# Kernel tuning notes

Measured on AMD Instinct MI355X. Metric: run time of the kernel, lower is better.

## Reference

```python
import jax, jax.numpy as jnp
import numpy as np

N_EMBD = 1024
N_HEAD = 16
HEAD_DIM = N_EMBD // N_HEAD
BLOCK_SIZE = 2048
ROPE_BASE = 10000.0


def _rope_tables(dim, max_len, base=ROPE_BASE):
    half = dim // 2
    freqs = 1.0 / base ** (jnp.arange(half, dtype=jnp.float32) / half)
    angles = jnp.arange(max_len, dtype=jnp.float32)[:, None] * freqs[None, :]  # (T, half)
    return jnp.cos(angles), jnp.sin(angles)


def _apply_rope(x, cos, sin):
    # x: (B, H, T, D); cos/sin: (T, D//2)
    T = x.shape[2]
    c = cos[:T][None, None]
    s = sin[:T][None, None]
    x1 = x[..., ::2]
    x2 = x[..., 1::2]
    out = jnp.stack([x1 * c - x2 * s, x1 * s + x2 * c], axis=-1)  # (B,H,T,D//2,2)
    return out.reshape(x.shape)


def setup_inputs() -> dict:
    key = jax.random.key(0)
    k1, k2, k3, k4, k5 = jax.random.split(key, 5)
    B, T, C = 2, 2048, N_EMBD
    x = jax.random.normal(k1, (B, T, C), dtype=jnp.float32)
    scale = 1.0 / np.sqrt(C)
    Wqkv = jax.random.normal(k2, (C, 3 * C), dtype=jnp.float32) * scale
    bqkv = jax.random.normal(k3, (3 * C,), dtype=jnp.float32) * 0.01
    Wproj = jax.random.normal(k4, (C, C), dtype=jnp.float32) * scale
    bproj = jax.random.normal(k5, (C,), dtype=jnp.float32) * 0.01
    cos, sin = _rope_tables(HEAD_DIM, BLOCK_SIZE)
    return {"x": x, "Wqkv": Wqkv, "bqkv": bqkv, "Wproj": Wproj, "bproj": bproj,
            "cos": cos, "sin": sin}


def reference(x, Wqkv, bqkv, Wproj, bproj, cos, sin):
    B, T, C = x.shape
    H, D = N_HEAD, HEAD_DIM
    qkv = x @ Wqkv + bqkv  # (B,T,3C)
    q, k, v = jnp.split(qkv, 3, axis=-1)
    # (B,T,C) -> (B,H,T,D)
    q = q.reshape(B, T, H, D).transpose(0, 2, 1, 3)
    k = k.reshape(B, T, H, D).transpose(0, 2, 1, 3)
    v = v.reshape(B, T, H, D).transpose(0, 2, 1, 3)
    q = _apply_rope(q, cos, sin)
    k = _apply_rope(k, cos, sin)
    att = jnp.einsum('bhtd,bhsd->bhts', q, k) * (D ** -0.5)
    causal = jnp.tril(jnp.ones((T, T), dtype=bool))
    att = jnp.where(causal[None, None], att, -jnp.inf)
    att = jax.nn.softmax(att, axis=-1)
    y = jnp.einsum('bhts,bhsd->bhtd', att, v)  # (B,H,T,D)
    y = y.transpose(0, 2, 1, 3).reshape(B, T, C)
    return y @ Wproj + bproj
```

## Files before the change

kernel.cpp:

```cpp
#include <hip/hip_runtime.h>
#include <stdint.h>

typedef short s16x8 __attribute__((ext_vector_type(8)));
typedef float f32x4 __attribute__((ext_vector_type(4)));
typedef unsigned short u16;
typedef unsigned int u32;

__device__ __forceinline__ float bf2f(u16 u) {
  union { u32 i; float f; } v; v.i = ((u32)u) << 16; return v.f;
}
__device__ __forceinline__ u16 f2bf(float f) {
  union { float f; u32 i; } v; v.f = f;
  u32 i = v.i;
  return (u16)((i + 0x7fffu + ((i >> 16) & 1u)) >> 16);
}
__device__ __forceinline__ u16 f2bf_fast(float f) {
  union { float f; u32 i; } v; v.f = f;
  return (u16)((v.i + 0x8000u) >> 16);
}

__device__ __forceinline__ s16x8 load8(const void* p, size_t idx, int isf32) {
  s16x8 r;
  if (isf32) {
    const float* f = (const float*)p + idx;
    f32x4 a = *(const f32x4*)f;
    f32x4 b = *(const f32x4*)(f + 4);
#pragma unroll
    for (int j = 0; j < 4; j++) {
      r[j] = (short)f2bf(a[j]);
      r[4 + j] = (short)f2bf(b[j]);
    }
  } else {
    r = *(const s16x8*)((const u16*)p + idx);
  }
  return r;
}
__device__ __forceinline__ float loadf(const void* p, size_t idx, int isf32) {
  return isf32 ? ((const float*)p)[idx] : bf2f(((const u16*)p)[idx]);
}

__device__ __forceinline__ void cp16(const u16* g, u16* l) {
  __builtin_amdgcn_global_load_lds(
      (const __attribute__((address_space(1))) u32*)g,
      (__attribute__((address_space(3))) u32*)l, 16, 0, 0);
}

__global__ void detect_dtype(const u16* __restrict__ x, int* __restrict__ flags) {
  int cnt = 0;
  for (int i = threadIdx.x; i < 4096; i += 64) {
    int e = (x[i] >> 7) & 0xFF;
    if (e >= 0xF0) cnt++;
  }
  unsigned long long any = __ballot(cnt > 0);
  if (threadIdx.x == 0) {
    flags[0] = (any != 0ull) ? 1 : 0;
    flags[1] = 0;
  }
}

__global__ __launch_bounds__(256) void convert_x(const void* __restrict__ x,
                                                 const int* __restrict__ fp,
                                                 u16* __restrict__ xb) {
  int tid = blockIdx.x * 256 + threadIdx.x;
  int r = tid & 127, kq = (tid >> 7) & 3, kB = (tid >> 9) & 31, mB = tid >> 14;
  size_t src = (size_t)(mB * 128 + r) * 1024 + kB * 32 + kq * 8;
  *(s16x8*)(xb + (size_t)tid * 8) = load8(x, src, *fp);
}

__global__ __launch_bounds__(256) void transposeW2(
    const void* __restrict__ Wqkv, const void* __restrict__ Wproj,
    const int* __restrict__ fp, u16* __restrict__ WqkvT,
    u16* __restrict__ WprojT) {
  __shared__ u32 tile32[32 * 66];
  const int f = *fp;
  const int tid = threadIdx.x;
  const int bx = blockIdx.x;
  const void* W;
  u16* WT;
  int N, nb, qkvSide;
  if (bx < 48) { W = Wqkv; WT = WqkvT; N = 3072; nb = bx * 64; qkvSide = 1; }
  else         { W = Wproj; WT = WprojT; N = 1024; nb = (bx - 48) * 64; qkvSide = 0; }
  const int kb = blockIdx.y * 64;
  {
    int a = tid >> 3, c8 = tid & 7;
    s16x8 r0 = load8(W, (size_t)(kb + 2 * a) * N + nb + c8 * 8, f);
    s16x8 r1 = load8(W, (size_t)(kb + 2 * a + 1) * N + nb + c8 * 8, f);
#pragma unroll
    for (int j = 0; j < 8; j++)
      tile32[a * 66 + c8 * 8 + j] = (u32)(u16)r0[j] | ((u32)(u16)r1[j] << 16);
  }
  __syncthreads();
#pragma unroll
  for (int i = 0; i < 2; i++) {
    int idx = tid + i * 256;
    int n = idx & 63, c8 = idx >> 6;
    s16x8 v;
#pragma unroll
    for (int w = 0; w < 4; w++) {
      u32 pk = tile32[(c8 * 4 + w) * 66 + n];
      v[2 * w] = (short)(u16)(pk & 0xFFFF);
      v[2 * w + 1] = (short)(u16)(pk >> 16);
    }
    int R = nb + n, k = kb + c8 * 8;
    int kB = k >> 5, kq = (k >> 3) & 3;
    size_t off;
    if (qkvSide) {
      int nB = R >> 7, r = R & 127;
      off = ((size_t)(nB * 32 + kB) * 4 + kq) * 1024 + r * 8;
    } else {
      int nB = R >> 6, r = R & 63;
      off = (size_t)(nB * 32 + kB) * 2048 + kq * 512 + r * 8;
    }
    *(s16x8*)(WT + off) = v;
  }
}

__global__ __launch_bounds__(256) void transposeV(const u16* __restrict__ qkv,
                                                  u16* __restrict__ vT) {
  __shared__ u32 tile32[64 * 33];
  const int tid = threadIdx.x;
  const int tb = blockIdx.x * 64, bh = blockIdx.y;
  const int b = bh >> 4, h = bh & 15;
  {
    int a = tid >> 3, c8 = tid & 7;
    const u16* base = qkv + (size_t)(b * 2048 + tb + 2 * a) * 3072 + 2048 + h * 64;
    s16x8 r0 = *(const s16x8*)(base + c8 * 8);
    s16x8 r1 = *(const s16x8*)(base + 3072 + c8 * 8);
#pragma unroll
    for (int j = 0; j < 8; j++)
      tile32[(c8 * 8 + j) * 33 + a] = (u32)(u16)r0[j] | ((u32)(u16)r1[j] << 16);
  }
  __syncthreads();
#pragma unroll
  for (int i = 0; i < 2; i++) {
    int idx = tid + i * 256;
    int d = idx >> 3, c8 = idx & 7;
    s16x8 v;
#pragma unroll
    for (int w = 0; w < 4; w++) {
      u32 pk = tile32[d * 33 + c8 * 4 + w];
      v[2 * w] = (short)(u16)(pk & 0xFFFF);
      v[2 * w + 1] = (short)(u16)(pk >> 16);
    }
    *(s16x8*)(vT + ((size_t)bh * 64 + d) * 2048 + tb + c8 * 8) = v;
  }
}

template <int MB, int NT, int KK, int ATILED>
__global__ __launch_bounds__(256, 6) void gemm_bt(
    const u16* __restrict__ A, int lda, const u16* __restrict__ Bt,
    const void* __restrict__ bias, const int* __restrict__ fI32,
    void* __restrict__ C, int ropeMode, int outF,
    const void* __restrict__ cost, const void* __restrict__ sint, int N) {
  constexpr int MT = MB / 32;
  constexpr int NTW = NT / 32;
  constexpr int KT = KK / 32;
  constexpr int APW = MB / 64;
  constexpr int BPW = NT / 64;
  __shared__ __attribute__((aligned(16))) u16 As[MB * 32];
  __shared__ __attribute__((aligned(16))) u16 Bs[NT * 32];
  const int inf32 = *fI32;
  const int tid = threadIdx.x;
  const int wave = tid >> 6, lane = tid & 63, quad = lane >> 4, l16 = lane & 15;
  const int bx = blockIdx.x, by = blockIdx.y;
  const int m0 = by * MB, n0 = bx * NT;
  const int wm = (wave & 1) * (MB / 2), wn = (wave >> 1) * (NT / 2);
  f32x4 acc[MT][NTW];
#pragma unroll
  for (int i = 0; i < MT; i++)
#pragma unroll
    for (int j = 0; j < NTW; j++) acc[i][j] = (f32x4){0.f, 0.f, 0.f, 0.f};

  const u16* aT = nullptr;
  const u16* aP = nullptr;
  int halfA = 0;
  if constexpr (ATILED) {
    const int mB = (MB == 128) ? by : (by >> 1);
    halfA = (MB == 128) ? 0 : (by & 1);
    aT = A + (size_t)mB * KK * 128 + lane * 8;
  } else {
    const int lr = lane >> 2, lk = (lane & 3) * 8;
    aP = A + (size_t)(m0 + wave * (MB / 4) + lr) * lda + lk;
  }
  const u16* bT = Bt + (size_t)bx * KK * NT + lane * 8;

  for (int s = 0; s < KT; ++s) {
    __syncthreads();
    if constexpr (ATILED) {
#pragma unroll
      for (int j = 0; j < APW; j++) {
        const int c = wave * APW + j;
        size_t off;
        if constexpr (MB == 128) off = (size_t)s * 4096 + c * 512;
        else                     off = (size_t)s * 4096 + c * 1024 + halfA * 512;
        cp16(aT + off, As + c * 512);
      }
    } else {
      const int kb = s * 32;
#pragma unroll
      for (int j = 0; j < APW; j++)
        cp16(aP + kb + (size_t)(16 * j) * lda, As + wave * (APW * 512) + j * 512);
    }
#pragma unroll
    for (int j = 0; j < BPW; j++) {
      const int c = wave * BPW + j;
      cp16(bT + (size_t)s * (NT * 32) + c * 512, Bs + c * 512);
    }
    __syncthreads();
    s16x8 af[MT], bfr[NTW];
#pragma unroll
    for (int mt = 0; mt < MT; mt++) {
      if constexpr (ATILED)
        af[mt] = *(const s16x8*)(As + quad * (MB * 8) + (wm + mt * 16 + l16) * 8);
      else
        af[mt] = *(const s16x8*)(As + (wm + mt * 16 + l16) * 32 + quad * 8);
    }
#pragma unroll
    for (int nt = 0; nt < NTW; nt++)
      bfr[nt] = *(const s16x8*)(Bs + quad * (NT * 8) + (wn + nt * 16 + l16) * 8);
#pragma unroll
    for (int mt = 0; mt < MT; mt++)
#pragma unroll
      for (int nt = 0; nt < NTW; nt++)
        acc[mt][nt] = __builtin_amdgcn_mfma_f32_16x16x32_bf16(
            af[mt], bfr[nt], acc[mt][nt], 0, 0, 0);
  }

#pragma unroll
  for (int nt = 0; nt < NTW; nt++) {
    int col = n0 + wn + nt * 16 + l16;
    float bv = loadf(bias, col, inf32);
    if (ropeMode && col < 2048) {
      int j = (col & 63) >> 1, odd = col & 1;
#pragma unroll
      for (int mt = 0; mt < MT; mt++)
#pragma unroll
        for (int r = 0; r < 4; r++) {
          int row = m0 + wm + mt * 16 + quad * 4 + r, t = row & 2047;
          float cv = loadf(cost, (size_t)t * 32 + j, inf32);
          float sv = loadf(sint, (size_t)t * 32 + j, inf32);
          float val = acc[mt][nt][r] + bv;
          float pr = __shfl_xor(val, 1);
          float res = odd ? (pr * sv + val * cv) : (val * cv - pr * sv);
          ((u16*)C)[(size_t)row * N + col] = f2bf(res);
        }
    } else if (outF && inf32) {
#pragma unroll
      for (int mt = 0; mt < MT; mt++)
#pragma unroll
        for (int r = 0; r < 4; r++) {
          int row = m0 + wm + mt * 16 + quad * 4 + r;
          ((float*)C)[(size_t)row * N + col] = acc[mt][nt][r] + bv;
        }
    } else {
#pragma unroll
      for (int mt = 0; mt < MT; mt++)
#pragma unroll
        for (int r = 0; r < 4; r++) {
          int row = m0 + wm + mt * 16 + quad * 4 + r;
          ((u16*)C)[(size_t)row * N + col] = f2bf(acc[mt][nt][r] + bv);
        }
    }
  }
}

__device__ __forceinline__ int kvIdx(int chunk, int row) {
  return chunk * 512 + (((row & 56) | ((row ^ chunk) & 7)) << 3);
}
__device__ __forceinline__ int pIdx(int chunk, int row) {
  return chunk * 128 + (((row & 8) | ((row ^ chunk) & 7)) << 3);
}

__global__ __launch_bounds__(512) void attn_kernel(u16* qkv,
                                                   const u16* __restrict__ vT) {
  __shared__ __attribute__((aligned(16))) u16 Ks[8 * 512];
  __shared__ __attribute__((aligned(16))) u16 Vt[8 * 512];
  __shared__ __attribute__((aligned(16))) u16 Pl[8][8 * 128];
  const int tid = threadIdx.x;
  const int wave = tid >> 6, lane = tid & 63, quad = lane >> 4, l16 = lane & 15;
  const int cu = blockIdx.x & 255, round = blockIdx.x >> 8;
  const int p = cu >> 5, bh = cu & 31;
  const int qt = round ? p : 15 - p;
  const int h = bh & 15;
  const size_t rb = (size_t)(bh >> 4) * 2048;
  const int qb = qt * 128;
  const float SCALE = 0.18033688011112042f;

  s16x8 qa0, qa1;
  {
    const u16* qp = qkv + (rb + qb + wave * 16 + l16) * 3072 + h * 64;
    qa0 = *(const s16x8*)(qp + quad * 8);
    qa1 = *(const s16x8*)(qp + 32 + quad * 8);
  }

  f32x4 o[4];
  float l_r[4] = {0.f, 0.f, 0.f, 0.f};
#pragma unroll
  for (int i = 0; i < 4; i++) o[i] = (f32x4){0.f, 0.f, 0.f, 0.f};

  const int nchunks = 2 * qt + 2;
  const int srow = tid >> 3, sc8 = tid & 7;
  const int stIdx = kvIdx(sc8, srow);
  s16x8 kr, vr;
  {
    kr = *(const s16x8*)(qkv + (rb + srow) * 3072 + 1024 + h * 64 + sc8 * 8);
    vr = *(const s16x8*)(vT + ((size_t)bh * 64 + srow) * 2048 + sc8 * 8);
  }

  for (int c = 0; c < nchunks; c++) {
    const int sb = c * 64;
    __syncthreads();
    *(s16x8*)(Ks + stIdx) = kr;
    *(s16x8*)(Vt + stIdx) = vr;
    __syncthreads();
    if (c + 1 < nchunks) {
      const int nb = sb + 64;
      kr = *(const s16x8*)(qkv + (rb + nb + srow) * 3072 + 1024 + h * 64 +
                           sc8 * 8);
      vr = *(const s16x8*)(vT + ((size_t)bh * 64 + srow) * 2048 + nb + sc8 * 8);
    }

    if (sb > qb + wave * 16 + 15) continue;

    f32x4 S[4];
#pragma unroll
    for (int kf = 0; kf < 4; kf++) {
      s16x8 k0 = *(const s16x8*)(Ks + kvIdx(quad, kf * 16 + l16));
      s16x8 k1 = *(const s16x8*)(Ks + kvIdx(quad + 4, kf * 16 + l16));
      f32x4 a = (f32x4){0.f, 0.f, 0.f, 0.f};
      a = __builtin_amdgcn_mfma_f32_16x16x32_bf16(qa0, k0, a, 0, 0, 0);
      a = __builtin_amdgcn_mfma_f32_16x16x32_bf16(qa1, k1, a, 0, 0, 0);
      S[kf] = a;
    }

    u16* P = Pl[wave];
    const int mq = qb + wave * 16;
    const bool needMask = (sb + 63) > mq;
#pragma unroll
    for (int r = 0; r < 4; r++) {
      const int qi = mq + quad * 4 + r;
#pragma unroll
      for (int kf = 0; kf < 4; kf++) {
        float pv = __builtin_amdgcn_exp2f(S[kf][r] * SCALE);
        if (needMask) pv = ((sb + kf * 16 + l16) <= qi) ? pv : 0.f;
        l_r[r] += pv;
        P[pIdx(kf * 2 + (l16 >> 3), quad * 4 + r) + (l16 & 7)] = f2bf_fast(pv);
      }
    }
    asm volatile("s_waitcnt lgkmcnt(0)" ::: "memory");
    s16x8 pa0 = *(const s16x8*)(P + pIdx(quad, l16));
    s16x8 pa1 = *(const s16x8*)(P + pIdx(quad + 4, l16));

#pragma unroll
    for (int dt = 0; dt < 4; dt++) {
      s16x8 vb0 = *(const s16x8*)(Vt + kvIdx(quad, dt * 16 + l16));
      s16x8 vb1 = *(const s16x8*)(Vt + kvIdx(quad + 4, dt * 16 + l16));
      o[dt] = __builtin_amdgcn_mfma_f32_16x16x32_bf16(pa0, vb0, o[dt], 0, 0, 0);
      o[dt] = __builtin_amdgcn_mfma_f32_16x16x32_bf16(pa1, vb1, o[dt], 0, 0, 0);
    }
  }

  float inv[4];
#pragma unroll
  for (int r = 0; r < 4; r++) {
    float rs = l_r[r];
#pragma unroll
    for (int off = 8; off; off >>= 1) rs += __shfl_xor(rs, off);
    inv[r] = 1.0f / fmaxf(rs, 1e-30f);
  }
#pragma unroll
  for (int dt = 0; dt < 4; dt++)
#pragma unroll
    for (int r = 0; r < 4; r++)
      qkv[(rb + qb + wave * 16 + quad * 4 + r) * 3072 + 2048 + h * 64 +
          dt * 16 + l16] = f2bf(o[dt][r] * inv[r]);
}

extern "C" void kernel_launch(void* const* d_in, const int* in_sizes, int n_in,
                              void* d_out, int out_size, void* d_ws,
                              size_t ws_size, hipStream_t stream) {
  const void* x = d_in[0];
  const void* Wqkv = d_in[1];
  const void* bqkv = d_in[2];
  const void* Wproj = d_in[3];
  const void* bproj = d_in[4];
  const void* cost = d_in[5];
  const void* sint = d_in[6];

  int* flags = (int*)d_ws;
  u16* WqkvT = (u16*)d_ws + 128;
  u16* WprojT = WqkvT + (size_t)3072 * 1024;
  u16* qkv = WprojT + (size_t)1024 * 1024;
  u16* yb = qkv + 2048;
  u16* xb = (u16*)d_out;
  u16* vT = (u16*)d_out + (size_t)4096 * 1024;

  detect_dtype<<<1, 64, 0, stream>>>((const u16*)x, flags);
  convert_x<<<2048, 256, 0, stream>>>(x, flags, xb);
  transposeW2<<<dim3(64, 16), 256, 0, stream>>>(Wqkv, Wproj, flags, WqkvT,
                                                WprojT);
  gemm_bt<64, 128, 1024, 1><<<dim3(24, 64), 256, 0, stream>>>(
      xb, 1024, WqkvT, bqkv, flags, qkv, 1, 0, cost, sint, 3072);
  transposeV<<<dim3(32, 32), 256, 0, stream>>>(qkv, vT);
  attn_kernel<<<512, 512, 0, stream>>>(qkv, vT);
  gemm_bt<64, 64, 1024, 0><<<dim3(16, 64), 256, 0, stream>>>(
      yb, 3072, WprojT, bproj, flags, d_out, 0, 1, nullptr, nullptr, 1024);
}
```

Baseline: 209.6 us.

## Split attention blocks into 64-query halves with double-buffered K/V staging

The attention kernel moves from 512-thread blocks covering 128 queries to 256-thread blocks covering 64 queries, with twice as many blocks. Each half-block only walks the key chunks it needs, so causal work per block is finer grained. K/V tiles are now double-buffered in shared memory with register prefetch two chunks ahead, which removes one barrier per iteration and overlaps global loads with MFMA work. In exchange, each block loads more K/V rows per thread and K/V is re-read from global memory by both query halves.

Result: no change. 213.0 us (+1.7%).

```diff
diff --git a/kernel.cpp b/kernel.cpp
--- a/kernel.cpp
+++ b/kernel.cpp
@@ -271,24 +271,26 @@
   return chunk * 128 + (((row & 8) | ((row ^ chunk) & 7)) << 3);
 }
 
-__global__ __launch_bounds__(512) void attn_kernel(u16* qkv,
-                                                   const u16* __restrict__ vT) {
-  __shared__ __attribute__((aligned(16))) u16 Ks[8 * 512];
-  __shared__ __attribute__((aligned(16))) u16 Vt[8 * 512];
-  __shared__ __attribute__((aligned(16))) u16 Pl[8][8 * 128];
+__global__ __launch_bounds__(256, 4) void attn_kernel(u16* qkv,
+                                                      const u16* __restrict__ vT) {
+  __shared__ __attribute__((aligned(16))) u16 Ks[2][8 * 512];
+  __shared__ __attribute__((aligned(16))) u16 Vt[2][8 * 512];
+  __shared__ __attribute__((aligned(16))) u16 Pl[4][8 * 128];
   const int tid = threadIdx.x;
   const int wave = tid >> 6, lane = tid & 63, quad = lane >> 4, l16 = lane & 15;
   const int cu = blockIdx.x & 255, round = blockIdx.x >> 8;
   const int p = cu >> 5, bh = cu & 31;
-  const int qt = round ? p : 15 - p;
+  const int qt = (round & 1) ? p : 15 - p;
+  const int half = 1 - (round >> 1);
   const int h = bh & 15;
   const size_t rb = (size_t)(bh >> 4) * 2048;
-  const int qb = qt * 128;
+  const int q0 = qt * 128 + half * 64;
+  const int mq = q0 + wave * 16;
   const float SCALE = 0.18033688011112042f;
 
   s16x8 qa0, qa1;
   {
-    const u16* qp = qkv + (rb + qb + wave * 16 + l16) * 3072 + h * 64;
+    const u16* qp = qkv + (rb + q0 + wave * 16 + l16) * 3072 + h * 64;
     qa0 = *(const s16x8*)(qp + quad * 8);
     qa1 = *(const s16x8*)(qp + 32 + quad * 8);
   }
@@ -298,66 +300,84 @@
 #pragma unroll
   for (int i = 0; i < 4; i++) o[i] = (f32x4){0.f, 0.f, 0.f, 0.f};
 
-  const int nchunks = 2 * qt + 2;
+  const int nchunks = 2 * qt + half + 1;
   const int srow = tid >> 3, sc8 = tid & 7;
-  const int stIdx = kvIdx(sc8, srow);
-  s16x8 kr, vr;
-  {
-    kr = *(const s16x8*)(qkv + (rb + srow) * 3072 + 1024 + h * 64 + sc8 * 8);
-    vr = *(const s16x8*)(vT + ((size_t)bh * 64 + srow) * 2048 + sc8 * 8);
-  }
+  const int si0 = kvIdx(sc8, srow), si1 = kvIdx(sc8, srow + 32);
+  const u16* kg = qkv + (rb + srow) * 3072 + 1024 + h * 64 + sc8 * 8;
+  const u16* vg = vT + ((size_t)bh * 64 + srow) * 2048 + sc8 * 8;
+
+  s16x8 kr0, kr1, vr0, vr1;
+  kr0 = *(const s16x8*)(kg);
+  kr1 = *(const s16x8*)(kg + (size_t)32 * 3072);
+  vr0 = *(const s16x8*)(vg);
+  vr1 = *(const s16x8*)(vg + (size_t)32 * 2048);
+  *(s16x8*)(&Ks[0][si0]) = kr0;
+  *(s16x8*)(&Ks[0][si1]) = kr1;
+  *(s16x8*)(&Vt[0][si0]) = vr0;
+  *(s16x8*)(&Vt[0][si1]) = vr1;
+  if (nchunks > 1) {
+    kr0 = *(const s16x8*)(kg + (size_t)64 * 3072);
+    kr1 = *(const s16x8*)(kg + (size_t)96 * 3072);
+    vr0 = *(const s16x8*)(vg + 64);
+    vr1 = *(const s16x8*)(vg + (size_t)32 * 2048 + 64);
+  }
+  __syncthreads();
 
   for (int c = 0; c < nchunks; c++) {
     const int sb = c * 64;
+    const int cur = c & 1;
+    if (c + 1 < nchunks) {
+      *(s16x8*)(&Ks[cur ^ 1][si0]) = kr0;
+      *(s16x8*)(&Ks[cur ^ 1][si1]) = kr1;
+      *(s16x8*)(&Vt[cur ^ 1][si0]) = vr0;
+      *(s16x8*)(&Vt[cur ^ 1][si1]) = vr1;
+      if (c + 2 < nchunks) {
+        const int nb = sb + 128;
+        kr0 = *(const s16x8*)(kg + (size_t)nb * 3072);
+        kr1 = *(const s16x8*)(kg + (size_t)(nb + 32) * 3072);
+        vr0 = *(const s16x8*)(vg + nb);
+        vr1 = *(const s16x8*)(vg + (size_t)32 * 2048 + nb);
+      }
+    }
+
+    if (sb <= mq + 15) {
+      f32x4 S[4];
+#pragma unroll
+      for (int kf = 0; kf < 4; kf++) {
+        s16x8 k0 = *(const s16x8*)(&Ks[cur][kvIdx(quad, kf * 16 + l16)]);
+        s16x8 k1 = *(const s16x8*)(&Ks[cur][kvIdx(quad + 4, kf * 16 + l16)]);
+        f32x4 a = (f32x4){0.f, 0.f, 0.f, 0.f};
+        a = __builtin_amdgcn_mfma_f32_16x16x32_bf16(qa0, k0, a, 0, 0, 0);
+        a = __builtin_amdgcn_mfma_f32_16x16x32_bf16(qa1, k1, a, 0, 0, 0);
+        S[kf] = a;
+      }
+
+      u16* P = Pl[wave];
+      const bool needMask = (sb + 63) > mq;
+#pragma unroll
+      for (int r = 0; r < 4; r++) {
+        const int qi = mq + quad * 4 + r;
+#pragma unroll
+        for (int kf = 0; kf < 4; kf++) {
+          float pv = __builtin_amdgcn_exp2f(S[kf][r] * SCALE);
+          if (needMask) pv = ((sb + kf * 16 + l16) <= qi) ? pv : 0.f;
+          l_r[r] += pv;
+          P[pIdx(kf * 2 + (l16 >> 3), quad * 4 + r) + (l16 & 7)] = f2bf_fast(pv);
+        }
+      }
+      asm volatile("s_waitcnt lgkmcnt(0)" ::: "memory");
+      s16x8 pa0 = *(const s16x8*)(P + pIdx(quad, l16));
+      s16x8 pa1 = *(const s16x8*)(P + pIdx(quad + 4, l16));
+
+#pragma unroll
+      for (int dt = 0; dt < 4; dt++) {
+        s16x8 vb0 = *(const s16x8*)(&Vt[cur][kvIdx(quad, dt * 16 + l16)]);
+        s16x8 vb1 = *(const s16x8*)(&Vt[cur][kvIdx(quad + 4, dt * 16 + l16)]);
+        o[dt] = __builtin_amdgcn_mfma_f32_16x16x32_bf16(pa0, vb0, o[dt], 0, 0, 0);
+        o[dt] = __builtin_amdgcn_mfma_f32_16x16x32_bf16(pa1, vb1, o[dt], 0, 0, 0);
+      }
+    }
     __syncthreads();
-    *(s16x8*)(Ks + stIdx) = kr;
-    *(s16x8*)(Vt + stIdx) = vr;
-    __syncthreads();
-    if (c + 1 < nchunks) {
-      const int nb = sb + 64;
-      kr = *(const s16x8*)(qkv + (rb + nb + srow) * 3072 + 1024 + h * 64 +
-                           sc8 * 8);
-      vr = *(const s16x8*)(vT + ((size_t)bh * 64 + srow) * 2048 + nb + sc8 * 8);
-    }
-
-    if (sb > qb + wave * 16 + 15) continue;
-
-    f32x4 S[4];
-#pragma unroll
-    for (int kf = 0; kf < 4; kf++) {
-      s16x8 k0 = *(const s16x8*)(Ks + kvIdx(quad, kf * 16 + l16));
-      s16x8 k1 = *(const s16x8*)(Ks + kvIdx(quad + 4, kf * 16 + l16));
-      f32x4 a = (f32x4){0.f, 0.f, 0.f, 0.f};
-      a = __builtin_amdgcn_mfma_f32_16x16x32_bf16(qa0, k0, a, 0, 0, 0);
-      a = __builtin_amdgcn_mfma_f32_16x16x32_bf16(qa1, k1, a, 0, 0, 0);
-      S[kf] = a;
-    }
-
-    u16* P = Pl[wave];
-    const int mq = qb + wave * 16;
-    const bool needMask = (sb + 63) > mq;
-#pragma unroll
-    for (int r = 0; r < 4; r++) {
-      const int qi = mq + quad * 4 + r;
-#pragma unroll
-      for (int kf = 0; kf < 4; kf++) {
-        float pv = __builtin_amdgcn_exp2f(S[kf][r] * SCALE);
-        if (needMask) pv = ((sb + kf * 16 + l16) <= qi) ? pv : 0.f;
-        l_r[r] += pv;
-        P[pIdx(kf * 2 + (l16 >> 3), quad * 4 + r) + (l16 & 7)] = f2bf_fast(pv);
-      }
-    }
-    asm volatile("s_waitcnt lgkmcnt(0)" ::: "memory");
-    s16x8 pa0 = *(const s16x8*)(P + pIdx(quad, l16));
-    s16x8 pa1 = *(const s16x8*)(P + pIdx(quad + 4, l16));
-
-#pragma unroll
-    for (int dt = 0; dt < 4; dt++) {
-      s16x8 vb0 = *(const s16x8*)(Vt + kvIdx(quad, dt * 16 + l16));
-      s16x8 vb1 = *(const s16x8*)(Vt + kvIdx(quad + 4, dt * 16 + l16));
-      o[dt] = __builtin_amdgcn_mfma_f32_16x16x32_bf16(pa0, vb0, o[dt], 0, 0, 0);
-      o[dt] = __builtin_amdgcn_mfma_f32_16x16x32_bf16(pa1, vb1, o[dt], 0, 0, 0);
-    }
   }
 
   float inv[4];
@@ -372,7 +392,7 @@
   for (int dt = 0; dt < 4; dt++)
 #pragma unroll
     for (int r = 0; r < 4; r++)
-      qkv[(rb + qb + wave * 16 + quad * 4 + r) * 3072 + 2048 + h * 64 +
+      qkv[(rb + mq + quad * 4 + r) * 3072 + 2048 + h * 64 +
           dt * 16 + l16] = f2bf(o[dt][r] * inv[r]);
 }
 
@@ -402,7 +422,7 @@
   gemm_bt<64, 128, 1024, 1><<<dim3(24, 64), 256, 0, stream>>>(
       xb, 1024, WqkvT, bqkv, flags, qkv, 1, 0, cost, sint, 3072);
   transposeV<<<dim3(32, 32), 256, 0, stream>>>(qkv, vT);
-  attn_kernel<<<512, 512, 0, stream>>>(qkv, vT);
+  attn_kernel<<<1024, 256, 0, stream>>>(qkv, vT);
   gemm_bt<64, 64, 1024, 0><<<dim3(16, 64), 256, 0, stream>>>(
       yb, 3072, WprojT, bproj, flags, d_out, 0, 1, nullptr, nullptr, 1024);
 }
```
